# Performance work log

Hardware: AMD Instinct MI355X
Metric: run time of the kernel (lower is better)

The kernel has to match this reference:

```python
import jax, jax.numpy as jnp
import numpy as np


def _operators_3_to_2(x2d, A, norm):
    # x2d: [b, d, n, n], A: [b, n, n]. Returns the 20 basis tensors, each [b, d, n, n].
    t = lambda a: a.transpose(0, 1, 3, 2)
    shape = x2d.shape
    op1 = jnp.einsum('bdij,bij,bik->bdjk', x2d, A, A) / norm
    op2 = jnp.einsum('bdij,bij,bjk->bdik', x2d, A, A) / norm
    op3 = jnp.einsum('bdij,bik,bjk->bdij', x2d, A, A) / norm
    op4 = jnp.broadcast_to(jnp.einsum('bdij,bij->bdi', x2d, A)[..., None], shape) / norm
    op5 = jnp.broadcast_to(jnp.einsum('bdij,bij->bdj', x2d, A)[..., None], shape) / norm
    op6 = jnp.einsum('bdij,bik->bdjk', x2d, A) / norm
    # NOTE: source has ops7 = [op6, op6.transpose] (bug: op7 computed but unused) -- replicated faithfully.
    op8 = jnp.einsum('bdij,bik->bdij', x2d, A) / norm
    op9 = jnp.einsum('bdij,bjk->bdij', x2d, A) / norm
    op10 = jnp.broadcast_to(x2d.sum(3, keepdims=True), shape) / norm
    op11 = jnp.broadcast_to(x2d.sum(2, keepdims=True), shape) / norm
    return [op1, t(op1), op2, t(op2), op3,
            op4, t(op4), op5, t(op5),
            op6, t(op6), op6, t(op6),
            op8, op9,
            op10, t(op10), op11, t(op11),
            x2d]


def _forward(x, edge_weight, coeffs1, bias1, coeffs2, bias2, edge_index, batch, n):
    f = x.shape[-1]
    b = x.shape[0] // n
    # to_2d_tensor: [b*n, f] -> [b, 2f, n, n]
    x2 = x.reshape(b, n, f).transpose(0, 2, 1)  # [b, f, n]
    x_2d = jnp.concatenate([
        jnp.broadcast_to(x2[:, :, :, None], (b, f, n, n)),
        jnp.broadcast_to(x2[:, :, None, :], (b, f, n, n)),
    ], axis=1)
    # to_dense_adj: scatter-add edge weights into per-graph dense [b, n, n]
    g = batch[edge_index[0]]
    r = edge_index[0] - g * n
    c = edge_index[1] - g * n
    A = jnp.zeros((b, n, n), x.dtype).at[g, r, c].add(edge_weight)
    norm = jnp.asarray(n, x.dtype)  # normalization=True default
    for li, (coeffs, bias) in enumerate([(coeffs1, bias1), (coeffs2, bias2)]):
        ops_out = jnp.stack(_operators_3_to_2(x_2d, A, norm), axis=2)  # [b, d, 20, n, n]
        x_2d = jnp.einsum('der,bdrij->beij', coeffs, ops_out) + bias
        if li == 0:
            x_2d = jax.nn.sigmoid(x_2d)
    return x_2d.mean(axis=(1, 2, 3))  # [b]


def setup_inputs() -> dict:
    key = jax.random.key(0)
    kx, kg, ks, kd, kw, kc1, kc2 = jax.random.split(key, 7)
    b, n, deg, f, h = 4, 128, 16, 32, 32
    d_in, d_out = 2 * f, 2 * h  # layer doubles channels; hidden layer is d_out -> d_out
    E = b * n * deg
    x = jax.random.normal(kx, (b * n, f), dtype=jnp.float32)
    g = jax.random.randint(kg, (E,), 0, b)
    src = jax.random.randint(ks, (E,), 0, n)
    dst = jax.random.randint(kd, (E,), 0, n)
    edge_index = jnp.stack([g * n + src, g * n + dst]).astype(jnp.int32)
    edge_weight = jax.random.uniform(kw, (E,), dtype=jnp.float32)
    batch = (jnp.arange(b * n) // n).astype(jnp.int32)
    scale1 = np.sqrt(2.0) / (d_in + d_out)
    scale2 = np.sqrt(2.0) / (d_out + d_out)
    coeffs1 = jax.random.normal(kc1, (d_in, d_out, 20), dtype=jnp.float32) * scale1
    coeffs2 = jax.random.normal(kc2, (d_out, d_out, 20), dtype=jnp.float32) * scale2
    bias1 = jnp.zeros((1, d_out, 1, 1), dtype=jnp.float32)
    bias2 = jnp.zeros((1, d_out, 1, 1), dtype=jnp.float32)
    return {"x": x, "edge_weight": edge_weight, "coeffs1": coeffs1, "bias1": bias1,
            "coeffs2": coeffs2, "bias2": bias2, "edge_index": edge_index,
            "batch": batch, "n": n}


def reference(x, edge_weight, coeffs1, bias1, coeffs2, bias2, edge_index, batch, n):
    return _forward(x, edge_weight, coeffs1, bias1, coeffs2, bias2, edge_index, batch, n)
```

## Files before the change

### kernel.cpp

```cpp
#include <hip/hip_runtime.h>
#include <stdint.h>

typedef unsigned short u16;
using short8 = __attribute__((ext_vector_type(8))) short;
using f32x4  = __attribute__((ext_vector_type(4))) float;

#define NB 4
#define NN 128
#define NF 32
#define ND 64
#define NMAT (NB*ND*NN*NN)

#define OFF_A     0u
#define OFF_ACC   262144u
#define OFF_AAT   262400u
#define OFF_RA    524544u
#define OFF_W     526592u
#define OFF_RM    1116416u
#define OFF_CM    1247488u
#define OFF_RX    1378560u
#define OFF_CX    1509632u
#define OFF_BF    1640960u
#define OFF_ATB   1641472u
#define OFF_WB    1772544u
#define OFF_X2    1936384u
#define OFF_XT    10324992u
#define OFF_UA    18713600u
#define OFF_UB    27102208u
#define OFF_UC    35490816u
#define OFF_UD    43879424u
#define OFF_YACC  52268032u
#define OFF_XF    (OFF_YACC)
#define OFF_EWF   (OFF_YACC + 65536u)
#define OFF_CF    (OFF_YACC + 98304u)

__device__ __forceinline__ float b2f(u16 v){
  union { uint32_t u; float f; } x; x.u = ((uint32_t)v) << 16; return x.f;
}
__device__ __forceinline__ u16 f2b(float f){
  union { uint32_t u; float f2; } x; x.f2 = f;
  uint32_t u = x.u;
  return (u16)((u + 0x7FFFu + ((u >> 16) & 1u)) >> 16);
}

#define MFMA16(a,b,c) __builtin_amdgcn_mfma_f32_16x16x32_bf16((a),(b),(c),0,0,0)

__device__ __constant__ signed char dR1[18] = {0,9,1,10,2,3,4,13,14,19,5,7,15,18,6,8,16,17};
__device__ __constant__ signed char dR2[18] = {-1,11,-1,12,-1,-1,-1,-1,-1,-1,-1,-1,-1,-1,-1,-1,-1,-1};

__global__ void k_convert(const void* __restrict__ xs, const void* __restrict__ ews,
                          const void* __restrict__ c1s, const void* __restrict__ c2s,
                          const void* __restrict__ b1s, const void* __restrict__ b2s,
                          float* __restrict__ xf, float* __restrict__ ewf,
                          float* __restrict__ cf, float* __restrict__ bfv){
  __shared__ int flg;
  const u16* x16 = (const u16*)xs;
  if (threadIdx.x == 0) flg = 0;
  __syncthreads();
  int hit = 0;
  for (int k = threadIdx.x; k < 1024; k += 256){
    u16 u = x16[k];
    if (((u >> 7) & 0xFF) >= 0x90) hit = 1;
  }
  if (hit) flg = 1;
  __syncthreads();
  const int isf = flg;

  int t = blockIdx.x*256 + threadIdx.x;
  if (t >= 188544) return;
  const void* src; int idx; float* dst;
  if (t < 16384)      { src = xs;  idx = t;          dst = xf + idx; }
  else if (t < 24576) { src = ews; idx = t - 16384;  dst = ewf + idx; }
  else if (t < 106496){ src = c1s; idx = t - 24576;  dst = cf + idx; }
  else if (t < 188416){ src = c2s; idx = t - 106496; dst = cf + 81920 + idx; }
  else if (t < 188480){ src = b1s; idx = t - 188416; dst = bfv + idx; }
  else                { src = b2s; idx = t - 188480; dst = bfv + 64 + idx; }
  float v = isf ? ((const float*)src)[idx] : b2f(((const u16*)src)[idx]);
  *dst = v;
}

__global__ void k_setup(const int* __restrict__ ei, const int* __restrict__ bat,
                        const float* __restrict__ ewf, float* __restrict__ A, int E,
                        const float* __restrict__ xf, u16* __restrict__ Xt,
                        const float* __restrict__ cf, float* __restrict__ W,
                        u16* __restrict__ Wb){
  const int bx = blockIdx.x;
  if (bx < 32){
    for (int t = bx*256 + threadIdx.x; t < E; t += 32*256){
      int s = ei[t], dnode = ei[E + t];
      int g = bat[s];
      int r = s - g*NN, c = dnode - g*NN;
      atomicAdd(&A[(g*NN + r)*NN + c], ewf[t]);
    }
  } else if (bx < 32 + 2048){
    int gid = (bx - 32)*256 + threadIdx.x;
    if (gid >= NMAT/8) return;
    int d0 = (gid & 7)*8;
    int ij = (gid >> 3) & 16383;
    int b  = gid >> 17;
    int i = ij >> 7, j = ij & 127;
    const float* src = (d0 < NF) ? &xf[(b*NN + i)*NF + d0] : &xf[(b*NN + j)*NF + (d0 - NF)];
    float4 f0 = *(const float4*)src;
    float4 f1 = *(const float4*)(src + 4);
    short8 v;
    v[0]=(short)f2b(f0.x); v[1]=(short)f2b(f0.y); v[2]=(short)f2b(f0.z); v[3]=(short)f2b(f0.w);
    v[4]=(short)f2b(f1.x); v[5]=(short)f2b(f1.y); v[6]=(short)f2b(f1.z); v[7]=(short)f2b(f1.w);
    *(short8*)(Xt + ((size_t)(b*16384 + ij))*64 + d0) = v;
  } else {
    int gl = (bx - 2080)*256 + threadIdx.x;
    if (gl >= 2*1152*64) return;
    int L = gl / (1152*64);
    int rem = gl - L*1152*64;
    int row = rem >> 6, e = rem & 63;
    int slot = row >> 6, d = row & 63;
    const float* cc = cf + L*81920;
    int base = (d*64 + e)*20;
    float v = cc[base + dR1[slot]];
    if (dR2[slot] >= 0) v += cc[base + dR2[slot]];
    float scale = (slot == 9) ? 1.0f : (1.0f/128.0f);
    v *= scale;
    W[gl] = v;
    if (slot < 10)
      Wb[(((size_t)L*10 + slot)*64 + e)*64 + d] = f2b(v);
  }
}

__global__ __launch_bounds__(256) void k_prepA(const float* __restrict__ A, float* __restrict__ AAt,
                                               u16* __restrict__ ATb, float* __restrict__ rA){
  const int iq = blockIdx.x, b = blockIdx.y;
  const int t = threadIdx.x;
  if (iq < 8){
    int j = t & 127, ih = t >> 7;
    const float* Ab = A + b*NN*NN;
    float acc[8] = {0,0,0,0,0,0,0,0};
    for (int k = 0; k < NN; k++){
      float aj = Ab[j*NN + k];
      #pragma unroll
      for (int ii = 0; ii < 8; ii++){
        int i = iq*16 + ih*8 + ii;
        acc[ii] += Ab[i*NN + k] * aj;
      }
    }
    #pragma unroll
    for (int ii = 0; ii < 8; ii++){
      int i = iq*16 + ih*8 + ii;
      AAt[(b*NN + i)*NN + j] = acc[ii];
    }
  } else if (iq == 8){
    __shared__ float lds[128][129];
    for (int l = 0; l < 64; l++){
      int idx = l*256 + t;
      lds[idx >> 7][idx & 127] = A[b*16384 + idx];
    }
    __syncthreads();
    for (int l = 0; l < 64; l++){
      int idx = l*256 + t;
      int r = idx >> 7, c = idx & 127;
      ATb[b*16384 + idx] = f2b(lds[c][r]);
    }
  } else {
    if (t < 128){
      const float* Ab = A + (b*NN + t)*NN;
      float s = 0.f;
      for (int j = 0; j < NN; j++) s += Ab[j];
      rA[b*NN + t] = s;
    }
  }
}

__global__ __launch_bounds__(256) void k_xt(const u16* __restrict__ X, u16* __restrict__ Xt){
  int b = blockIdx.y;
  int ij0 = blockIdx.x*64;
  __shared__ u16 lds[64][65];
  int t = threadIdx.x;
  #pragma unroll
  for (int l = 0; l < 2; l++){
    int idx = l*2048 + t*8;
    int d = idx >> 6, c = idx & 63;
    const u16* p = X + ((size_t)(b*64 + d))*16384 + ij0 + c;
    short8 v = *(const short8*)p;
    #pragma unroll
    for (int k = 0; k < 8; k++) lds[d][c + k] = (u16)v[k];
  }
  __syncthreads();
  #pragma unroll
  for (int l = 0; l < 2; l++){
    int idx = l*2048 + t*8;
    int r = idx >> 6, c = idx & 63;
    short8 v;
    #pragma unroll
    for (int k = 0; k < 8; k++) v[k] = (short)lds[c + k][r];
    *(short8*)(Xt + ((size_t)(b*16384 + ij0 + r))*64 + c) = v;
  }
}

#define SJ32 72
#define SJF  69

__global__ __launch_bounds__(256) void k_mixrow(const u16* __restrict__ Xt, const float* __restrict__ A,
    const float* __restrict__ AAt, const float* __restrict__ rA, const u16* __restrict__ Wb,
    u16* __restrict__ Ua, u16* __restrict__ Ub, u16* __restrict__ Uc, u16* __restrict__ Ud,
    float* __restrict__ Yacc,
    float* __restrict__ RM, float* __restrict__ CM,
    float* __restrict__ RX, float* __restrict__ CXv)
{
  const int b = blockIdx.y;
  const int t = threadIdx.x;

  if (blockIdx.x >= 256){
    int d = t & 63;
    int task = (blockIdx.x - 256)*4 + (t >> 6);
    float sm = 0.f, sx = 0.f;
    if (task < 128){
      int i = task;
      for (int j = 0; j < 128; j++){
        float xv = b2f(Xt[((size_t)(b*16384 + i*128 + j))*64 + d]);
        float av = A[b*16384 + i*128 + j];
        sm += xv*av; sx += xv;
      }
      RM[(b*64 + d)*128 + i] = sm;
      RX[(b*64 + d)*128 + i] = sx;
    } else {
      int j = task - 128;
      for (int i = 0; i < 128; i++){
        float xv = b2f(Xt[((size_t)(b*16384 + i*128 + j))*64 + d]);
        float av = A[b*16384 + i*128 + j];
        sm += xv*av; sx += xv;
      }
      CM[(b*64 + d)*128 + j] = sm;
      CXv[(b*64 + d)*128 + j] = sx;
    }
    return;
  }

  const int w = t >> 6, lane = t & 63;
  const int col = lane & 15, quad = lane >> 4;
  const int ij0 = blockIdx.x*64;

  __shared__ uint32_t lsb[4][32*SJ32];
  __shared__ float lsf[64*SJF];

  short8 wa[10][2];
  #pragma unroll
  for (int s = 0; s < 10; s++){
    const u16* wp = Wb + (size_t)((s*64 + w*16 + col)*64 + quad*8);
    wa[s][0] = *(const short8*)wp;
    wa[s][1] = *(const short8*)(wp + 32);
  }
  short8 xb[4][2];
  #pragma unroll
  for (int sj = 0; sj < 4; sj++){
    const u16* xp = Xt + ((size_t)(b*16384 + ij0 + sj*16 + col))*64 + quad*8;
    xb[sj][0] = *(const short8*)xp;
    xb[sj][1] = *(const short8*)(xp + 32);
  }
  float a_s[4], t_s[4], rjv[4];
  #pragma unroll
  for (int sj = 0; sj < 4; sj++){
    int ij = ij0 + sj*16 + col;
    a_s[sj] = A[b*16384 + ij];
    t_s[sj] = AAt[b*16384 + ij];
    rjv[sj] = rA[b*128 + (ij & 127)];
  }
  const float riv = rA[b*128 + (ij0 >> 7)];

  #pragma unroll
  for (int g = 0; g < 5; g++){
    const int s0_tab[5]  = {0, 2, 4, 5, 6};
    const int nsl_tab[5] = {2, 2, 1, 1, 4};
    const int s0 = s0_tab[g], nsl = nsl_tab[g];
    #pragma unroll
    for (int sj = 0; sj < 4; sj++){
      f32x4 acc[4];
      #pragma unroll
      for (int s = 0; s < 4; s++) acc[s] = (f32x4){0.f,0.f,0.f,0.f};
      #pragma unroll
      for (int s = 0; s < 4; s++){
        if (s >= nsl) break;
        acc[s] = MFMA16(wa[s0+s][0], xb[sj][0], acc[s]);
        acc[s] = MFMA16(wa[s0+s][1], xb[sj][1], acc[s]);
      }
      if (g < 4){
        float v[4];
        #pragma unroll
        for (int r = 0; r < 4; r++){
          if (g == 2 || g == 3) v[r] = acc[0][r]*a_s[sj];
          else                  v[r] = acc[0][r]*a_s[sj] + acc[1][r];
        }
        uint32_t p0 = (uint32_t)f2b(v[0]) | ((uint32_t)f2b(v[1]) << 16);
        uint32_t p1 = (uint32_t)f2b(v[2]) | ((uint32_t)f2b(v[3]) << 16);
        int ep = w*8 + quad*2;
        lsb[g][ep*SJ32 + sj*16 + col] = p0;
        lsb[g][(ep + 1)*SJ32 + sj*16 + col] = p1;
      } else {
        #pragma unroll
        for (int r = 0; r < 4; r++){
          float v = acc[0][r]*t_s[sj] + acc[1][r]*riv + acc[2][r]*rjv[sj] + acc[3][r];
          lsf[(w*16 + quad*4 + r)*SJF + sj*16 + col] = v;
        }
      }
    }
  }
  __syncthreads();

  const int eo = t >> 2, seg = t & 3;
  const int ep = eo >> 1, sh = (eo & 1)*16;
  #pragma unroll
  for (int g = 0; g < 4; g++){
    const uint32_t* lp = &lsb[g][ep*SJ32 + seg*16];
    short8 v0, v1;
    #pragma unroll
    for (int k = 0; k < 8; k++){
      v0[k] = (short)((lp[k]   >> sh) & 0xffffu);
      v1[k] = (short)((lp[8+k] >> sh) & 0xffffu);
    }
    u16* U = (g==0)?Ua:(g==1)?Ub:(g==2)?Uc:Ud;
    u16* dst = U + ((size_t)(b*64 + eo) << 14) + ij0 + seg*16;
    *(short8*)dst = v0;
    *(short8*)(dst + 8) = v1;
  }
  {
    const float* fp = &lsf[eo*SJF + seg*16];
    float* dst = Yacc + ((size_t)(b*64 + eo) << 14) + ij0 + seg*16;
    #pragma unroll
    for (int q = 0; q < 4; q++)
      *(float4*)(dst + q*4) = make_float4(fp[q*4], fp[q*4+1], fp[q*4+2], fp[q*4+3]);
  }
}

#define SLT 68

__global__ __launch_bounds__(256) void k_tne(const u16* __restrict__ ATb,
    const u16* __restrict__ Ua, const u16* __restrict__ Ub,
    const u16* __restrict__ Uc, const u16* __restrict__ Ud,
    const float* __restrict__ Yacc, const float* __restrict__ W,
    const float* __restrict__ RM, const float* __restrict__ CM,
    const float* __restrict__ RX, const float* __restrict__ CXv,
    const float* __restrict__ bias, u16* __restrict__ Xout, float* __restrict__ acc4, int last)
{
  const int nh = blockIdx.x, be = blockIdx.y;
  const int b = be >> 6, e = be & 63;
  const int t = threadIdx.x, wave = t >> 6, lane = t & 63;
  const int col = lane & 15, quad = lane >> 4;
  const int m0 = (wave >> 1)*64;
  const int n0 = nh*64 + (wave & 1)*32;
  const int nb0 = nh*64;

  __shared__ uint32_t uls[128*SLT];
  __shared__ uint32_t ubl[64*SLT];
  __shared__ float radd[128], cadd[128];
  __shared__ float red[4];

  if (t < 128){
    int i = t; float s = 0.f;
    for (int d = 0; d < ND; d++){
      int v = (b*ND + d)*NN + i;
      s += W[(640 + d)*64 + e]*RM[v] + W[(704 + d)*64 + e]*CM[v]
         + W[(768 + d)*64 + e]*RX[v] + W[(832 + d)*64 + e]*CXv[v];
    }
    radd[i] = s;
  } else {
    int j = t - 128; float s = 0.f;
    for (int d = 0; d < ND; d++){
      int v = (b*ND + d)*NN + j;
      s += W[(896 + d)*64 + e]*RM[v] + W[(960 + d)*64 + e]*CM[v]
         + W[(1024 + d)*64 + e]*RX[v] + W[(1088 + d)*64 + e]*CXv[v];
    }
    cadd[j] = s;
  }

  const u16* ua = Ua + ((size_t)be << 14);
  const u16* ub = Ub + ((size_t)be << 14);
  {
    const int kp = t >> 2;
    #pragma unroll
    for (int it = 0; it < 4; it++){
      int mo = it*4 + (t & 3);
      short8 r0 = *(const short8*)(ua + (2*kp)*128 + mo*8);
      short8 r1 = *(const short8*)(ua + (2*kp + 1)*128 + mo*8);
      #pragma unroll
      for (int x = 0; x < 8; x++)
        uls[(mo*8 + x)*SLT + kp] = ((uint32_t)(u16)r0[x]) | (((uint32_t)(u16)r1[x]) << 16);
    }
    #pragma unroll
    for (int it = 0; it < 2; it++){
      int no = it*4 + (t & 3);
      short8 r0 = *(const short8*)(ub + (2*kp)*128 + nb0 + no*8);
      short8 r1 = *(const short8*)(ub + (2*kp + 1)*128 + nb0 + no*8);
      #pragma unroll
      for (int x = 0; x < 8; x++)
        ubl[(no*8 + x)*SLT + kp] = ((uint32_t)(u16)r0[x]) | (((uint32_t)(u16)r1[x]) << 16);
    }
  }
  __syncthreads();

  f32x4 acc[4][2];
  #pragma unroll
  for (int mt = 0; mt < 4; mt++)
    #pragma unroll
    for (int nt = 0; nt < 2; nt++)
      acc[mt][nt] = (f32x4){0.f,0.f,0.f,0.f};

  const u16* at = ATb + ((size_t)b << 14);
  short8 at_n[4][2];
  #pragma unroll
  for (int kq = 0; kq < 4; kq++){
    int k0 = kq*32 + quad*8;
    at_n[kq][0] = *(const short8*)(at + (n0 + col)*128 + k0);
    at_n[kq][1] = *(const short8*)(at + (n0 + 16 + col)*128 + k0);
  }

  #pragma unroll
  for (int kq = 0; kq < 4; kq++){
    int kd = kq*16 + quad*4;
    #pragma unroll
    for (int mt = 0; mt < 4; mt++){
      short8 af = *(const short8*)&uls[(m0 + mt*16 + col)*SLT + kd];
      acc[mt][0] = MFMA16(af, at_n[kq][0], acc[mt][0]);
      acc[mt][1] = MFMA16(af, at_n[kq][1], acc[mt][1]);
    }
  }
  #pragma unroll
  for (int kq = 0; kq < 4; kq++){
    int k0 = kq*32 + quad*8, kd = kq*16 + quad*4;
    short8 bf0 = *(const short8*)&ubl[((wave & 1)*32 + 0*16 + col)*SLT + kd];
    short8 bf1 = *(const short8*)&ubl[((wave & 1)*32 + 1*16 + col)*SLT + kd];
    #pragma unroll
    for (int mt = 0; mt < 4; mt++){
      short8 af = *(const short8*)(at + (m0 + mt*16 + col)*128 + k0);
      acc[mt][0] = MFMA16(af, bf0, acc[mt][0]);
      acc[mt][1] = MFMA16(af, bf1, acc[mt][1]);
    }
  }
  {
    const u16* uc = Uc + ((size_t)be << 14);
    #pragma unroll
    for (int kq = 0; kq < 4; kq++){
      int k0 = kq*32 + quad*8;
      #pragma unroll
      for (int mt = 0; mt < 4; mt++){
        short8 af = *(const short8*)(uc + (m0 + mt*16 + col)*128 + k0);
        acc[mt][0] = MFMA16(af, at_n[kq][0], acc[mt][0]);
        acc[mt][1] = MFMA16(af, at_n[kq][1], acc[mt][1]);
      }
    }
  }
  {
    const u16* ud = Ud + ((size_t)be << 14);
    #pragma unroll
    for (int kq = 0; kq < 4; kq++){
      int k0 = kq*32 + quad*8;
      short8 bf0 = *(const short8*)(ud + (n0 + col)*128 + k0);
      short8 bf1 = *(const short8*)(ud + (n0 + 16 + col)*128 + k0);
      #pragma unroll
      for (int mt = 0; mt < 4; mt++){
        short8 af = *(const short8*)(at + (m0 + mt*16 + col)*128 + k0);
        acc[mt][0] = MFMA16(af, bf0, acc[mt][0]);
        acc[mt][1] = MFMA16(af, bf1, acc[mt][1]);
      }
    }
  }
  __syncthreads();

  uint32_t* stg = uls;
  const float bv = bias[e];
  const float* Y = Yacc + ((size_t)be << 14);
  if (!last){
    #pragma unroll
    for (int mt = 0; mt < 4; mt++)
      #pragma unroll
      for (int nt = 0; nt < 2; nt++)
        #pragma unroll
        for (int rp = 0; rp < 2; rp++){
          uint32_t p = 0;
          #pragma unroll
          for (int h = 0; h < 2; h++){
            int r = rp*2 + h;
            int row = m0 + mt*16 + quad*4 + r;
            int cn = n0 + nt*16 + col;
            float v = acc[mt][nt][r] + Y[row*128 + cn] + radd[row] + cadd[cn] + bv;
            v = 1.f/(1.f + __expf(-v));
            p |= ((uint32_t)f2b(v)) << (16*h);
          }
          int ipair = (m0 + mt*16 + quad*4) >> 1;
          stg[(ipair + rp)*SLT + (wave & 1)*32 + nt*16 + col] = p;
        }
    __syncthreads();
    const uint32_t* lp = &stg[(t >> 2)*SLT + (t & 1)*32];
    const int sh = ((t >> 1) & 1)*16;
    u16* dst = Xout + ((size_t)be << 14) + (size_t)(t >> 1)*128 + nh*64 + (t & 1)*32;
    #pragma unroll
    for (int q2 = 0; q2 < 4; q2++){
      short8 v;
      #pragma unroll
      for (int k = 0; k < 8; k++) v[k] = (short)((lp[q2*8 + k] >> sh) & 0xffffu);
      *(short8*)(dst + q2*8) = v;
    }
  } else {
    float loc = 0.f;
    #pragma unroll
    for (int mt = 0; mt < 4; mt++)
      #pragma unroll
      for (int nt = 0; nt < 2; nt++)
        #pragma unroll
        for (int r = 0; r < 4; r++){
          int row = m0 + mt*16 + quad*4 + r;
          int cn = n0 + nt*16 + col;
          loc += acc[mt][nt][r] + Y[row*128 + cn] + radd[row] + cadd[cn] + bv;
        }
    for (int off = 32; off > 0; off >>= 1) loc += __shfl_down(loc, off, 64);
    if (lane == 0) red[wave] = loc;
    __syncthreads();
    if (t == 0) atomicAdd(&acc4[b], red[0] + red[1] + red[2] + red[3]);
  }
}

__global__ void k_finish(const float* __restrict__ acc4, const u16* __restrict__ x16,
                         void* __restrict__ out){
  __shared__ int flg;
  int t = threadIdx.x;
  if (t == 0) flg = 0;
  __syncthreads();
  int hit = 0;
  for (int k = t; k < 512; k += 64){
    u16 u = x16[k];
    if (((u >> 7) & 0xFF) >= 0x90) hit = 1;
  }
  if (hit) flg = 1;
  __syncthreads();
  if (t < NB){
    float v = acc4[t] * (1.0f/1048576.0f);
    if (flg) ((float*)out)[t] = v;
    else     ((u16*)out)[t] = f2b(v);
  }
}

extern "C" void kernel_launch(void* const* d_in, const int* in_sizes, int n_in,
                              void* d_out, int out_size, void* d_ws, size_t ws_size,
                              hipStream_t stream)
{
  const void* x   = d_in[0];
  const void* ew  = d_in[1];
  const void* c1  = d_in[2];
  const void* b1  = d_in[3];
  const void* c2  = d_in[4];
  const void* b2  = d_in[5];
  const int* ei  = (const int*)d_in[6];
  const int* bat = (const int*)d_in[7];
  const int E = in_sizes[1];

  char* wsb = (char*)d_ws;
  float* A    = (float*)(wsb + OFF_A);
  float* acc4 = (float*)(wsb + OFF_ACC);
  float* AAt  = (float*)(wsb + OFF_AAT);
  float* rA   = (float*)(wsb + OFF_RA);
  float* W    = (float*)(wsb + OFF_W);
  float* RM   = (float*)(wsb + OFF_RM);
  float* CM   = (float*)(wsb + OFF_CM);
  float* RX   = (float*)(wsb + OFF_RX);
  float* CXv  = (float*)(wsb + OFF_CX);
  float* bfv  = (float*)(wsb + OFF_BF);
  u16* ATb = (u16*)(wsb + OFF_ATB);
  u16* Wb  = (u16*)(wsb + OFF_WB);
  u16* X2  = (u16*)(wsb + OFF_X2);
  u16* Xt  = (u16*)(wsb + OFF_XT);
  u16* Ua  = (u16*)(wsb + OFF_UA);
  u16* Ub  = (u16*)(wsb + OFF_UB);
  u16* Uc  = (u16*)(wsb + OFF_UC);
  u16* Ud  = (u16*)(wsb + OFF_UD);
  float* Yacc = (float*)(wsb + OFF_YACC);
  float* xf   = (float*)(wsb + OFF_XF);
  float* ewf  = (float*)(wsb + OFF_EWF);
  float* cf   = (float*)(wsb + OFF_CF);

  hipMemsetAsync(wsb, 0, OFF_AAT, stream);

  k_convert<<<dim3(737), dim3(256), 0, stream>>>(x, ew, c1, c2, b1, b2, xf, ewf, cf, bfv);
  k_setup<<<dim3(2656), dim3(256), 0, stream>>>(ei, bat, ewf, A, E, xf, Xt, cf, W, Wb);
  k_prepA<<<dim3(10, NB), dim3(256), 0, stream>>>(A, AAt, ATb, rA);

  for (int L = 0; L < 2; L++){
    const float* Wl = W + (size_t)L*1152*64;
    const u16*  Wbl = Wb + (size_t)L*10*64*64;
    if (L == 1)
      k_xt<<<dim3(256, NB), dim3(256), 0, stream>>>(X2, Xt);
    k_mixrow<<<dim3(320, NB), dim3(256), 0, stream>>>(Xt, A, AAt, rA, Wbl,
                                                      Ua, Ub, Uc, Ud, Yacc, RM, CM, RX, CXv);
    k_tne<<<dim3(2, 256), dim3(256), 0, stream>>>(ATb, Ua, Ub, Uc, Ud, Yacc, Wl,
                                                  RM, CM, RX, CXv, bfv + L*64, X2, acc4, L);
  }
  k_finish<<<dim3(1), dim3(64), 0, stream>>>(acc4, (const u16*)x, d_out);
}
```

Before: 236.5 us.

## Keep activations in channel-major layout and transpose in LDS inside mixrow

Activations now stay in a single [b][d][ij] bf16 buffer. The setup kernel writes the initial tensor in that layout, and the row/column reductions index it directly. The separate k_xt transpose kernel and its extra global buffer are removed; k_mixrow instead loads a 64x64 tile with coalesced reads and transposes it through a padded LDS array before the MFMA loads. This removes one launch and a full global read/write pass per layer, at the cost of extra LDS use and a block barrier in k_mixrow.

```diff
diff --git a/kernel.cpp b/kernel.cpp
--- a/kernel.cpp
+++ b/kernel.cpp
@@ -23,8 +23,7 @@
 #define OFF_BF    1640960u
 #define OFF_ATB   1641472u
 #define OFF_WB    1772544u
-#define OFF_X2    1936384u
-#define OFF_XT    10324992u
+#define OFF_XB    1936384u
 #define OFF_UA    18713600u
 #define OFF_UB    27102208u
 #define OFF_UC    35490816u
@@ -81,7 +80,7 @@
 
 __global__ void k_setup(const int* __restrict__ ei, const int* __restrict__ bat,
                         const float* __restrict__ ewf, float* __restrict__ A, int E,
-                        const float* __restrict__ xf, u16* __restrict__ Xt,
+                        const float* __restrict__ xf, u16* __restrict__ XB,
                         const float* __restrict__ cf, float* __restrict__ W,
                         u16* __restrict__ Wb){
   const int bx = blockIdx.x;
@@ -95,17 +94,21 @@
   } else if (bx < 32 + 2048){
     int gid = (bx - 32)*256 + threadIdx.x;
     if (gid >= NMAT/8) return;
-    int d0 = (gid & 7)*8;
-    int ij = (gid >> 3) & 16383;
+    int c8 = gid & 2047;
+    int ij0 = c8*8;
+    int e  = (gid >> 11) & 63;
     int b  = gid >> 17;
-    int i = ij >> 7, j = ij & 127;
-    const float* src = (d0 < NF) ? &xf[(b*NN + i)*NF + d0] : &xf[(b*NN + j)*NF + (d0 - NF)];
-    float4 f0 = *(const float4*)src;
-    float4 f1 = *(const float4*)(src + 4);
+    int i = ij0 >> 7, j0 = ij0 & 127;
     short8 v;
-    v[0]=(short)f2b(f0.x); v[1]=(short)f2b(f0.y); v[2]=(short)f2b(f0.z); v[3]=(short)f2b(f0.w);
-    v[4]=(short)f2b(f1.x); v[5]=(short)f2b(f1.y); v[6]=(short)f2b(f1.z); v[7]=(short)f2b(f1.w);
-    *(short8*)(Xt + ((size_t)(b*16384 + ij))*64 + d0) = v;
+    if (e < NF){
+      u16 s = f2b(xf[(b*NN + i)*NF + e]);
+      #pragma unroll
+      for (int x = 0; x < 8; x++) v[x] = (short)s;
+    } else {
+      #pragma unroll
+      for (int x = 0; x < 8; x++) v[x] = (short)f2b(xf[(b*NN + j0 + x)*NF + (e - NF)]);
+    }
+    *(short8*)(XB + ((size_t)(b*64 + e) << 14) + ij0) = v;
   } else {
     int gl = (bx - 2080)*256 + threadIdx.x;
     if (gl >= 2*1152*64) return;
@@ -168,36 +171,11 @@
   }
 }
 
-__global__ __launch_bounds__(256) void k_xt(const u16* __restrict__ X, u16* __restrict__ Xt){
-  int b = blockIdx.y;
-  int ij0 = blockIdx.x*64;
-  __shared__ u16 lds[64][65];
-  int t = threadIdx.x;
-  #pragma unroll
-  for (int l = 0; l < 2; l++){
-    int idx = l*2048 + t*8;
-    int d = idx >> 6, c = idx & 63;
-    const u16* p = X + ((size_t)(b*64 + d))*16384 + ij0 + c;
-    short8 v = *(const short8*)p;
-    #pragma unroll
-    for (int k = 0; k < 8; k++) lds[d][c + k] = (u16)v[k];
-  }
-  __syncthreads();
-  #pragma unroll
-  for (int l = 0; l < 2; l++){
-    int idx = l*2048 + t*8;
-    int r = idx >> 6, c = idx & 63;
-    short8 v;
-    #pragma unroll
-    for (int k = 0; k < 8; k++) v[k] = (short)lds[c + k][r];
-    *(short8*)(Xt + ((size_t)(b*16384 + ij0 + r))*64 + c) = v;
-  }
-}
-
 #define SJ32 72
 #define SJF  69
-
-__global__ __launch_bounds__(256) void k_mixrow(const u16* __restrict__ Xt, const float* __restrict__ A,
+#define SXT  72
+
+__global__ __launch_bounds__(256) void k_mixrow(const u16* __restrict__ XB, const float* __restrict__ A,
     const float* __restrict__ AAt, const float* __restrict__ rA, const u16* __restrict__ Wb,
     u16* __restrict__ Ua, u16* __restrict__ Ub, u16* __restrict__ Uc, u16* __restrict__ Ud,
     float* __restrict__ Yacc,
@@ -210,11 +188,12 @@
   if (blockIdx.x >= 256){
     int d = t & 63;
     int task = (blockIdx.x - 256)*4 + (t >> 6);
+    const u16* Xb_ = XB + ((size_t)(b*64 + d) << 14);
     float sm = 0.f, sx = 0.f;
     if (task < 128){
       int i = task;
       for (int j = 0; j < 128; j++){
-        float xv = b2f(Xt[((size_t)(b*16384 + i*128 + j))*64 + d]);
+        float xv = b2f(Xb_[i*128 + j]);
         float av = A[b*16384 + i*128 + j];
         sm += xv*av; sx += xv;
       }
@@ -223,7 +202,7 @@
     } else {
       int j = task - 128;
       for (int i = 0; i < 128; i++){
-        float xv = b2f(Xt[((size_t)(b*16384 + i*128 + j))*64 + d]);
+        float xv = b2f(Xb_[i*128 + j]);
         float av = A[b*16384 + i*128 + j];
         sm += xv*av; sx += xv;
       }
@@ -239,6 +218,7 @@
 
   __shared__ uint32_t lsb[4][32*SJ32];
   __shared__ float lsf[64*SJF];
+  __shared__ u16 xtl[64*SXT];
 
   short8 wa[10][2];
   #pragma unroll
@@ -247,13 +227,19 @@
     wa[s][0] = *(const short8*)wp;
     wa[s][1] = *(const short8*)(wp + 32);
   }
-  short8 xb[4][2];
-  #pragma unroll
-  for (int sj = 0; sj < 4; sj++){
-    const u16* xp = Xt + ((size_t)(b*16384 + ij0 + sj*16 + col))*64 + quad*8;
-    xb[sj][0] = *(const short8*)xp;
-    xb[sj][1] = *(const short8*)(xp + 32);
-  }
+
+  {
+    const int e = t >> 2, c2 = (t & 3)*2;
+    const u16* xr = XB + ((size_t)(b*64 + e) << 14) + ij0;
+    #pragma unroll
+    for (int cc = 0; cc < 2; cc++){
+      int c = c2 + cc;
+      short8 v = *(const short8*)(xr + c*8);
+      #pragma unroll
+      for (int x = 0; x < 8; x++) xtl[(c*8 + x)*SXT + e] = (u16)v[x];
+    }
+  }
+
   float a_s[4], t_s[4], rjv[4];
   #pragma unroll
   for (int sj = 0; sj < 4; sj++){
@@ -263,6 +249,16 @@
     rjv[sj] = rA[b*128 + (ij & 127)];
   }
   const float riv = rA[b*128 + (ij0 >> 7)];
+
+  __syncthreads();
+
+  short8 xb[4][2];
+  #pragma unroll
+  for (int sj = 0; sj < 4; sj++){
+    const u16* xp = &xtl[(sj*16 + col)*SXT + quad*8];
+    xb[sj][0] = *(const short8*)xp;
+    xb[sj][1] = *(const short8*)(xp + 32);
+  }
 
   #pragma unroll
   for (int g = 0; g < 5; g++){
@@ -562,8 +558,7 @@
   float* bfv  = (float*)(wsb + OFF_BF);
   u16* ATb = (u16*)(wsb + OFF_ATB);
   u16* Wb  = (u16*)(wsb + OFF_WB);
-  u16* X2  = (u16*)(wsb + OFF_X2);
-  u16* Xt  = (u16*)(wsb + OFF_XT);
+  u16* XB  = (u16*)(wsb + OFF_XB);
   u16* Ua  = (u16*)(wsb + OFF_UA);
   u16* Ub  = (u16*)(wsb + OFF_UB);
   u16* Uc  = (u16*)(wsb + OFF_UC);
@@ -576,18 +571,16 @@
   hipMemsetAsync(wsb, 0, OFF_AAT, stream);
 
   k_convert<<<dim3(737), dim3(256), 0, stream>>>(x, ew, c1, c2, b1, b2, xf, ewf, cf, bfv);
-  k_setup<<<dim3(2656), dim3(256), 0, stream>>>(ei, bat, ewf, A, E, xf, Xt, cf, W, Wb);
+  k_setup<<<dim3(2656), dim3(256), 0, stream>>>(ei, bat, ewf, A, E, xf, XB, cf, W, Wb);
   k_prepA<<<dim3(10, NB), dim3(256), 0, stream>>>(A, AAt, ATb, rA);
 
   for (int L = 0; L < 2; L++){
     const float* Wl = W + (size_t)L*1152*64;
     const u16*  Wbl = Wb + (size_t)L*10*64*64;
-    if (L == 1)
-      k_xt<<<dim3(256, NB), dim3(256), 0, stream>>>(X2, Xt);
-    k_mixrow<<<dim3(320, NB), dim3(256), 0, stream>>>(Xt, A, AAt, rA, Wbl,
+    k_mixrow<<<dim3(320, NB), dim3(256), 0, stream>>>(XB, A, AAt, rA, Wbl,
                                                       Ua, Ub, Uc, Ud, Yacc, RM, CM, RX, CXv);
     k_tne<<<dim3(2, 256), dim3(256), 0, stream>>>(ATb, Ua, Ub, Uc, Ud, Yacc, Wl,
-                                                  RM, CM, RX, CXv, bfv + L*64, X2, acc4, L);
+                                                  RM, CM, RX, CXv, bfv + L*64, XB, acc4, L);
   }
   k_finish<<<dim3(1), dim3(64), 0, stream>>>(acc4, (const u16*)x, d_out);
 }
```

New measurement: 297.0 us. 25.6% more time.
